# Optimization experiments

Measured on AMD Instinct MI355X. Metric: run time of the kernel, lower is better.

The kernel has to match this reference:

```python
import jax, jax.numpy as jnp
import numpy as np

B, L, D = 256, 2048, 128   # batch, events per stay, latent_dim
V = 6000                   # n_tokens
T_MAX = 48                 # number of 1.0-wide time bins (dt = 1.0)


def setup_inputs() -> dict:
    key = jax.random.key(0)
    k1, k2, k3, k4 = jax.random.split(key, 4)
    # channel 0: continuous event times in [0, 48); channel 1: token ids (1..V-1, 0 = pad)
    T = jax.random.uniform(k1, (B, L), minval=0.0, maxval=float(T_MAX))
    ids = jax.random.randint(k2, (B, L), 1, V)
    X = jnp.concatenate([T[..., None], ids.astype(jnp.float32)[..., None]], axis=-1)
    # truncnorm init as in Embedding.reset_parameters: std-normal truncated to [-t, t]
    t_x = 1.0 / np.sqrt(V)
    embX = jax.random.truncated_normal(k3, -t_x, t_x, (V, D), dtype=jnp.float32)
    embX = embX.at[0].set(0.0)  # nn.Embedding padding_idx=0 zeroes row 0
    t_w = 1.0 / np.sqrt(V + 1)
    embW = jax.random.truncated_normal(k4, -t_w, t_w, (V + 1, 1), dtype=jnp.float32)
    return {"X": X, "embX": embX, "embW": embW}


def reference(X, embX, embW):
    # X: (B, L, 2) -> times T and int token ids
    T = X[:, :, 0]
    ids = X[:, :, 1].astype(jnp.int32)
    emb = embX[ids]                 # (B, L, D)
    w = jnp.exp(embW[ids])          # (B, L, 1)
    vals = (w * emb).reshape(B * L, D)
    # loop over t with mask (t <= T) & (T < t+1), dt=1 -> bin = floor(T)
    bins = jnp.clip(jnp.floor(T).astype(jnp.int32), 0, T_MAX - 1)
    seg = (jnp.arange(B, dtype=jnp.int32)[:, None] * T_MAX + bins).reshape(-1)
    sums = jax.ops.segment_sum(vals, seg, num_segments=B * T_MAX)        # (B*T_MAX, D)
    counts = jax.ops.segment_sum(jnp.ones((B * L,), X.dtype), seg,
                                 num_segments=B * T_MAX)                  # (B*T_MAX,)
    out = sums / (counts[:, None] + 1e-6)
    return out.reshape(B, T_MAX, D)
```

## Files before the change

### kernel.cpp

```cpp
#include <hip/hip_runtime.h>

#define BB   256
#define LL   2048
#define DD   128
#define TMAX 48
#define BLOCK 1024
#define NWAVE (BLOCK / 64)

__global__ __launch_bounds__(BLOCK, 1) void embed_bin_kernel(
    const float* __restrict__ X,
    const float* __restrict__ embX,
    const float* __restrict__ embW,
    float* __restrict__ out)
{
    __shared__ float2 s_meta[LL];
    __shared__ float2 s_sorted[LL];
    __shared__ int    s_cnt[TMAX];
    __shared__ int    s_start[TMAX];
    __shared__ int    s_ofs[TMAX];

    const int b    = blockIdx.x;
    const int tid  = threadIdx.x;
    const int lane = tid & 63;
    const int wv   = tid >> 6;

    if (tid < TMAX) s_cnt[tid] = 0;
    __syncthreads();

    const float2* Xb = (const float2*)(X + (size_t)b * LL * 2);
    for (int l = tid; l < LL; l += BLOCK) {
        float2 x = Xb[l];
        int id  = (int)x.y;
        int bin = (int)x.x;
        bin = bin < 0 ? 0 : (bin > TMAX - 1 ? TMAX - 1 : bin);
        float w = __expf(embW[id]);
        float2 m;
        m.x = __int_as_float(id | (bin << 16));
        m.y = w;
        s_meta[l] = m;
        atomicAdd(&s_cnt[bin], 1);
    }
    __syncthreads();

    if (wv == 0) {
        int orig = (lane < TMAX) ? s_cnt[lane] : 0;
        int c = orig;
        #pragma unroll
        for (int d = 1; d < 64; d <<= 1) {
            int t = __shfl_up(c, d);
            if (lane >= d) c += t;
        }
        if (lane < TMAX) { s_start[lane] = c - orig; s_ofs[lane] = c - orig; }
    }
    __syncthreads();

    for (int l = tid; l < LL; l += BLOCK) {
        float2 m = s_meta[l];
        int bits = __float_as_int(m.x);
        int bin  = bits >> 16;
        int pos  = atomicAdd(&s_ofs[bin], 1);
        float2 sm;
        sm.x = __int_as_float(bits & 0xFFFF);
        sm.y = m.y;
        s_sorted[pos] = sm;
    }
    __syncthreads();

    const int col = lane << 1;
    for (int t = wv; t < TMAX; t += NWAVE) {
        const int start = s_start[t];
        const int n     = s_cnt[t];
        float2 a0 = {0.f, 0.f}, a1 = {0.f, 0.f}, a2 = {0.f, 0.f}, a3 = {0.f, 0.f};
        int i = 0;
        for (; i + 4 <= n; i += 4) {
            float2 m0 = s_sorted[start + i];
            float2 m1 = s_sorted[start + i + 1];
            float2 m2 = s_sorted[start + i + 2];
            float2 m3 = s_sorted[start + i + 3];
            float2 e0 = *(const float2*)(embX + __float_as_int(m0.x) * DD + col);
            float2 e1 = *(const float2*)(embX + __float_as_int(m1.x) * DD + col);
            float2 e2 = *(const float2*)(embX + __float_as_int(m2.x) * DD + col);
            float2 e3 = *(const float2*)(embX + __float_as_int(m3.x) * DD + col);
            a0.x = fmaf(m0.y, e0.x, a0.x); a0.y = fmaf(m0.y, e0.y, a0.y);
            a1.x = fmaf(m1.y, e1.x, a1.x); a1.y = fmaf(m1.y, e1.y, a1.y);
            a2.x = fmaf(m2.y, e2.x, a2.x); a2.y = fmaf(m2.y, e2.y, a2.y);
            a3.x = fmaf(m3.y, e3.x, a3.x); a3.y = fmaf(m3.y, e3.y, a3.y);
        }
        for (; i < n; ++i) {
            float2 m0 = s_sorted[start + i];
            float2 e0 = *(const float2*)(embX + __float_as_int(m0.x) * DD + col);
            a0.x = fmaf(m0.y, e0.x, a0.x); a0.y = fmaf(m0.y, e0.y, a0.y);
        }
        float sx = (a0.x + a1.x) + (a2.x + a3.x);
        float sy = (a0.y + a1.y) + (a2.y + a3.y);
        float c  = (float)n + 1e-6f;
        float2 r;
        r.x = sx / c;
        r.y = sy / c;
        *(float2*)(out + (size_t)b * TMAX * DD + t * DD + col) = r;
    }
}

extern "C" void kernel_launch(void* const* d_in, const int* in_sizes, int n_in,
                              void* d_out, int out_size, void* d_ws, size_t ws_size,
                              hipStream_t stream) {
    const float* X    = (const float*)d_in[0];
    const float* embX = (const float*)d_in[1];
    const float* embW = (const float*)d_in[2];
    float* out        = (float*)d_out;

    embed_bin_kernel<<<dim3(BB), dim3(BLOCK), 0, stream>>>(X, embX, embW, out);
}
```

Before: 80.54 us.

## Gather embeddings as float4 with half-wave token split and keep metadata in registers

The gather loop now has each half-wave handle a different token and each lane load a float4 of the embedding row. That halves the number of serial gather iterations per bin and widens each load. The halves are combined with a cross-lane shuffle before the single store. Token metadata is also kept in registers between the count and scatter phases instead of staging it in shared memory. In exchange, out-of-range tail slots are padded with zero weight, which adds wasted loads, and the final division becomes a multiply by a reciprocal.

```diff
diff --git a/kernel.cpp b/kernel.cpp
--- a/kernel.cpp
+++ b/kernel.cpp
@@ -6,6 +6,7 @@
 #define TMAX 48
 #define BLOCK 1024
 #define NWAVE (BLOCK / 64)
+#define TPT  (LL / BLOCK)
 
 __global__ __launch_bounds__(BLOCK, 1) void embed_bin_kernel(
     const float* __restrict__ X,
@@ -13,7 +14,6 @@
     const float* __restrict__ embW,
     float* __restrict__ out)
 {
-    __shared__ float2 s_meta[LL];
     __shared__ float2 s_sorted[LL];
     __shared__ int    s_cnt[TMAX];
     __shared__ int    s_start[TMAX];
@@ -28,16 +28,16 @@
     __syncthreads();
 
     const float2* Xb = (const float2*)(X + (size_t)b * LL * 2);
-    for (int l = tid; l < LL; l += BLOCK) {
-        float2 x = Xb[l];
+    int   tok_bits[TPT];
+    float tok_w[TPT];
+    #pragma unroll
+    for (int j = 0; j < TPT; ++j) {
+        float2 x = Xb[tid + j * BLOCK];
         int id  = (int)x.y;
         int bin = (int)x.x;
         bin = bin < 0 ? 0 : (bin > TMAX - 1 ? TMAX - 1 : bin);
-        float w = __expf(embW[id]);
-        float2 m;
-        m.x = __int_as_float(id | (bin << 16));
-        m.y = w;
-        s_meta[l] = m;
+        tok_bits[j] = id | (bin << 16);
+        tok_w[j]    = __expf(embW[id]);
         atomicAdd(&s_cnt[bin], 1);
     }
     __syncthreads();
@@ -54,50 +54,57 @@
     }
     __syncthreads();
 
-    for (int l = tid; l < LL; l += BLOCK) {
-        float2 m = s_meta[l];
-        int bits = __float_as_int(m.x);
-        int bin  = bits >> 16;
-        int pos  = atomicAdd(&s_ofs[bin], 1);
+    #pragma unroll
+    for (int j = 0; j < TPT; ++j) {
+        int bin = tok_bits[j] >> 16;
+        int pos = atomicAdd(&s_ofs[bin], 1);
         float2 sm;
-        sm.x = __int_as_float(bits & 0xFFFF);
-        sm.y = m.y;
+        sm.x = __int_as_float(tok_bits[j] & 0xFFFF);
+        sm.y = tok_w[j];
         s_sorted[pos] = sm;
     }
     __syncthreads();
 
-    const int col = lane << 1;
+    const int half = lane >> 5;
+    const int col4 = (lane & 31) << 2;
     for (int t = wv; t < TMAX; t += NWAVE) {
         const int start = s_start[t];
         const int n     = s_cnt[t];
-        float2 a0 = {0.f, 0.f}, a1 = {0.f, 0.f}, a2 = {0.f, 0.f}, a3 = {0.f, 0.f};
-        int i = 0;
-        for (; i + 4 <= n; i += 4) {
-            float2 m0 = s_sorted[start + i];
-            float2 m1 = s_sorted[start + i + 1];
-            float2 m2 = s_sorted[start + i + 2];
-            float2 m3 = s_sorted[start + i + 3];
-            float2 e0 = *(const float2*)(embX + __float_as_int(m0.x) * DD + col);
-            float2 e1 = *(const float2*)(embX + __float_as_int(m1.x) * DD + col);
-            float2 e2 = *(const float2*)(embX + __float_as_int(m2.x) * DD + col);
-            float2 e3 = *(const float2*)(embX + __float_as_int(m3.x) * DD + col);
-            a0.x = fmaf(m0.y, e0.x, a0.x); a0.y = fmaf(m0.y, e0.y, a0.y);
-            a1.x = fmaf(m1.y, e1.x, a1.x); a1.y = fmaf(m1.y, e1.y, a1.y);
-            a2.x = fmaf(m2.y, e2.x, a2.x); a2.y = fmaf(m2.y, e2.y, a2.y);
-            a3.x = fmaf(m3.y, e3.x, a3.x); a3.y = fmaf(m3.y, e3.y, a3.y);
+        float4 a0 = {0,0,0,0}, a1 = {0,0,0,0}, a2 = {0,0,0,0}, a3 = {0,0,0,0};
+        for (int i = 0; i < n; i += 8) {
+            float4 e[4];
+            float  w[4];
+            #pragma unroll
+            for (int j = 0; j < 4; ++j) {
+                int k = i + 2 * j + half;
+                bool valid = k < n;
+                float2 m = s_sorted[start + (valid ? k : 0)];
+                w[j] = valid ? m.y : 0.0f;
+                e[j] = *(const float4*)(embX + __float_as_int(m.x) * DD + col4);
+            }
+            a0.x = fmaf(w[0], e[0].x, a0.x); a0.y = fmaf(w[0], e[0].y, a0.y);
+            a0.z = fmaf(w[0], e[0].z, a0.z); a0.w = fmaf(w[0], e[0].w, a0.w);
+            a1.x = fmaf(w[1], e[1].x, a1.x); a1.y = fmaf(w[1], e[1].y, a1.y);
+            a1.z = fmaf(w[1], e[1].z, a1.z); a1.w = fmaf(w[1], e[1].w, a1.w);
+            a2.x = fmaf(w[2], e[2].x, a2.x); a2.y = fmaf(w[2], e[2].y, a2.y);
+            a2.z = fmaf(w[2], e[2].z, a2.z); a2.w = fmaf(w[2], e[2].w, a2.w);
+            a3.x = fmaf(w[3], e[3].x, a3.x); a3.y = fmaf(w[3], e[3].y, a3.y);
+            a3.z = fmaf(w[3], e[3].z, a3.z); a3.w = fmaf(w[3], e[3].w, a3.w);
         }
-        for (; i < n; ++i) {
-            float2 m0 = s_sorted[start + i];
-            float2 e0 = *(const float2*)(embX + __float_as_int(m0.x) * DD + col);
-            a0.x = fmaf(m0.y, e0.x, a0.x); a0.y = fmaf(m0.y, e0.y, a0.y);
+        float4 a;
+        a.x = (a0.x + a1.x) + (a2.x + a3.x);
+        a.y = (a0.y + a1.y) + (a2.y + a3.y);
+        a.z = (a0.z + a1.z) + (a2.z + a3.z);
+        a.w = (a0.w + a1.w) + (a2.w + a3.w);
+        a.x += __shfl_xor(a.x, 32);
+        a.y += __shfl_xor(a.y, 32);
+        a.z += __shfl_xor(a.z, 32);
+        a.w += __shfl_xor(a.w, 32);
+        if (half == 0) {
+            float inv = 1.0f / ((float)n + 1e-6f);
+            float4 r = { a.x * inv, a.y * inv, a.z * inv, a.w * inv };
+            *(float4*)(out + (size_t)b * TMAX * DD + t * DD + col4) = r;
         }
-        float sx = (a0.x + a1.x) + (a2.x + a3.x);
-        float sy = (a0.y + a1.y) + (a2.y + a3.y);
-        float c  = (float)n + 1e-6f;
-        float2 r;
-        r.x = sx / c;
-        r.y = sy / c;
-        *(float2*)(out + (size_t)b * TMAX * DD + t * DD + col) = r;
     }
 }
 
```

After: 75.02 us. -6.9%, faster.
